# Kernel optimization log

Measured on AMD Instinct MI355X. Metric: run time of the kernel, lower is better.

## Reference

```python
import jax, jax.numpy as jnp
import numpy as np

H, W, C = 192, 192, 1024

def setup_inputs() -> dict:
    key = jax.random.key(0)
    k1, k2 = jax.random.split(key)
    x = jax.random.normal(k1, (1, H, W, C), dtype=jnp.float32)
    gamma = jax.random.normal(k2, (1,), dtype=jnp.float32)
    return {"x": x, "gamma": gamma}

def reference(x, gamma):
    b, h, w, c = x.shape
    # NOTE: faithful to the TF code: a pure reshape of NHWC into (1, C, H*W),
    # with NO transpose (the original relies on reshape semantics).
    proj = x.reshape(1, c, h * w)                      # query == key^T == value
    energy = jnp.einsum('bcn,bdn->bcd', proj, proj)    # (1, C, C)
    energy_new = jnp.max(energy, axis=-1, keepdims=True) - energy  # sign-flipped
    attention = jax.nn.softmax(energy_new, axis=-1)    # (1, C, C)
    out = jnp.einsum('bcd,bdn->bcn', attention, proj)  # (1, C, H*W)
    out = out.reshape(1, h, w, c)
    return gamma * out + x
```

## Files before the change

### kernel.cpp

```cpp
#include <hip/hip_runtime.h>
#include <cstdint>

#define C_DIM 1024
#define N_DIM 36864

typedef unsigned short ushort_t;
typedef __attribute__((ext_vector_type(8))) short bf16x8;
typedef __attribute__((ext_vector_type(4))) float f32x4;

__device__ __forceinline__ ushort_t f2b(float f) {
    unsigned u = __float_as_uint(f);
    u = (u + 0x7fffu + ((u >> 16) & 1u)) >> 16;
    return (ushort_t)u;
}
__device__ __forceinline__ float b2f(ushort_t b) {
    return __uint_as_float(((unsigned)b) << 16);
}

__device__ __forceinline__ void async16(const void* g, const void* lds) {
    __builtin_amdgcn_global_load_lds(
        (const __attribute__((address_space(1))) unsigned int*)(uintptr_t)g,
        (__attribute__((address_space(3))) unsigned int*)(uint32_t)(uintptr_t)lds,
        16, 0, 0);
}

__global__ __launch_bounds__(256) void k_convert(const float* __restrict__ x,
                                                 ushort_t* __restrict__ ph,
                                                 ushort_t* __restrict__ pl) {
    int i = blockIdx.x * 256 + threadIdx.x;
    float4 v = ((const float4*)x)[i];
    ushort4 h, l;
    h.x = f2b(v.x); l.x = f2b(v.x - b2f(h.x));
    h.y = f2b(v.y); l.y = f2b(v.y - b2f(h.y));
    h.z = f2b(v.z); l.z = f2b(v.z - b2f(h.z));
    h.w = f2b(v.w); l.w = f2b(v.w - b2f(h.w));
    ((ushort4*)ph)[i] = h;
    ((ushort4*)pl)[i] = l;
}

__global__ __launch_bounds__(256) void k_convtrans(const float* __restrict__ x,
                                                   ushort_t* __restrict__ ph,
                                                   ushort_t* __restrict__ pl,
                                                   ushort_t* __restrict__ pht) {
    __shared__ __align__(16) ushort_t th[64][72];
    const int t = threadIdx.x;
    const int i = t >> 2, qd = t & 3;
    const int c0 = blockIdx.y << 6;
    const size_t n0 = (size_t)blockIdx.x << 6;

    const size_t row = (size_t)(c0 + i) * N_DIM + n0 + (qd << 4);
    const float* src = x + row;
    union { ushort_t s[16]; uint4 q[2]; } H, Lo;
#pragma unroll
    for (int u4 = 0; u4 < 4; ++u4) {
        float4 v = ((const float4*)src)[u4];
        ushort_t h0 = f2b(v.x), h1 = f2b(v.y), h2 = f2b(v.z), h3 = f2b(v.w);
        H.s[u4 * 4 + 0] = h0; Lo.s[u4 * 4 + 0] = f2b(v.x - b2f(h0));
        H.s[u4 * 4 + 1] = h1; Lo.s[u4 * 4 + 1] = f2b(v.y - b2f(h1));
        H.s[u4 * 4 + 2] = h2; Lo.s[u4 * 4 + 2] = f2b(v.z - b2f(h2));
        H.s[u4 * 4 + 3] = h3; Lo.s[u4 * 4 + 3] = f2b(v.w - b2f(h3));
    }
    *(uint4*)(ph + row)     = H.q[0];
    *(uint4*)(ph + row + 8) = H.q[1];
    *(uint4*)(pl + row)     = Lo.q[0];
    *(uint4*)(pl + row + 8) = Lo.q[1];
    *(uint4*)&th[i][qd << 4]       = H.q[0];
    *(uint4*)&th[i][(qd << 4) + 8] = H.q[1];
    __syncthreads();

    ushort_t tmp[16];
#pragma unroll
    for (int u = 0; u < 16; ++u) tmp[u] = th[(qd << 4) + u][i];
    ushort_t* dst = pht + (n0 + i) * C_DIM + c0 + (qd << 4);
    *(uint4*)dst       = *(uint4*)tmp;
    *(uint4*)(dst + 8) = *(uint4*)(tmp + 8);
}

__global__ __launch_bounds__(256) void k_egemm(const ushort_t* __restrict__ ph,
                                               const ushort_t* __restrict__ pl,
                                               float* __restrict__ g1,
                                               float* __restrict__ g2,
                                               int kchunk) {
    __shared__ __align__(16) ushort_t sA [2][128 * 32];
    __shared__ __align__(16) ushort_t sBh[2][64 * 32];
    __shared__ __align__(16) ushort_t sBl[2][64 * 32];

    const int t = threadIdx.x;
    const int w = t >> 6;
    const int L = t & 63;
    const int c0 = blockIdx.x << 7;
    const int d0 = blockIdx.y << 6;
    const int kb = blockIdx.z * kchunk;
    const int lrow = L >> 2, lcol = (L & 3) << 3;

    const ushort_t* gA0 = ph + (size_t)(c0 + (w << 5) + lrow) * N_DIM + kb + lcol;
    const ushort_t* gB0 = (w < 2 ? ph : pl) +
                          (size_t)(d0 + ((w & 1) << 5) + lrow) * N_DIM + kb + lcol;
    ushort_t* lA[2] = { sA[0] + ((w << 5) << 5), sA[1] + ((w << 5) << 5) };
    ushort_t* lB[2] = { (w < 2 ? sBh[0] : sBl[0]) + (((w & 1) << 5) << 5),
                        (w < 2 ? sBh[1] : sBl[1]) + (((w & 1) << 5) << 5) };

    const int wm = (w >> 1) << 6;
    const int wn = (w & 1) << 5;
    const int lm = L & 15, q = L >> 4;

    f32x4 acc1[4][2], acc2[4][2];
#pragma unroll
    for (int a = 0; a < 4; ++a)
#pragma unroll
        for (int b = 0; b < 2; ++b) { acc1[a][b] = (f32x4)0.0f; acc2[a][b] = (f32x4)0.0f; }

    auto stage = [&](int ti, int b) {
        const ushort_t* ga = gA0 + (ti << 5);
        const ushort_t* gb = gB0 + (ti << 5);
        async16(ga,              lA[b]);
        async16(ga + 16 * N_DIM, lA[b] + 16 * 32);
        async16(gb,              lB[b]);
        async16(gb + 16 * N_DIM, lB[b] + 16 * 32);
    };

    const int nIter = kchunk >> 5;
    stage(0, 0);

    for (int ti = 0; ti < nIter; ++ti) {
        const int cb = ti & 1;
        if (ti + 1 < nIter) {
            stage(ti + 1, cb ^ 1);
            __builtin_amdgcn_s_waitcnt(0x0F74);
        } else {
            __builtin_amdgcn_s_waitcnt(0x0F70);
        }
        __builtin_amdgcn_s_barrier();

        bf16x8 a[4], bh[2], bl[2];
#pragma unroll
        for (int mt = 0; mt < 4; ++mt)
            a[mt] = *(const bf16x8*)(sA[cb] + ((wm + (mt << 4) + lm) << 5) + (q << 3));
#pragma unroll
        for (int nt = 0; nt < 2; ++nt) {
            bh[nt] = *(const bf16x8*)(sBh[cb] + ((wn + (nt << 4) + lm) << 5) + (q << 3));
            bl[nt] = *(const bf16x8*)(sBl[cb] + ((wn + (nt << 4) + lm) << 5) + (q << 3));
        }
#pragma unroll
        for (int mt = 0; mt < 4; ++mt)
#pragma unroll
            for (int nt = 0; nt < 2; ++nt) {
                acc1[mt][nt] = __builtin_amdgcn_mfma_f32_16x16x32_bf16(a[mt], bh[nt], acc1[mt][nt], 0, 0, 0);
                acc2[mt][nt] = __builtin_amdgcn_mfma_f32_16x16x32_bf16(a[mt], bl[nt], acc2[mt][nt], 0, 0, 0);
            }
        __builtin_amdgcn_s_barrier();
    }

    const size_t zb = (size_t)blockIdx.z << 20;
#pragma unroll
    for (int mt = 0; mt < 4; ++mt)
#pragma unroll
        for (int nt = 0; nt < 2; ++nt)
#pragma unroll
            for (int r = 0; r < 4; ++r) {
                int cg = c0 + wm + (mt << 4) + (q << 2) + r;
                int dg = d0 + wn + (nt << 4) + lm;
                size_t o = zb + ((size_t)cg << 10) + dg;
                g1[o] = acc1[mt][nt][r];
                g2[o] = acc2[mt][nt][r];
            }
}

__global__ __launch_bounds__(256) void k_reduce(const float* __restrict__ g1,
                                                const float* __restrict__ g2,
                                                float* __restrict__ E,
                                                int splitk) {
    __shared__ float ld[64][65];
    const int t = threadIdx.x;
    const int i = t >> 2;
    const int jb = (t & 3) << 4;
    const int c0 = blockIdx.y << 6;
    const int d0 = blockIdx.x << 6;

    float acc[16];
#pragma unroll
    for (int u = 0; u < 16; ++u) acc[u] = 0.0f;

    for (int z = 0; z < splitk; ++z) {
        const size_t zb = (size_t)z << 20;
        const float* p1 = g1 + zb + ((size_t)(c0 + i) << 10) + d0 + jb;
        const float* p2 = g2 + zb + ((size_t)(c0 + i) << 10) + d0 + jb;
        const float* pt = g2 + zb + ((size_t)(d0 + i) << 10) + c0 + jb;
#pragma unroll
        for (int u4 = 0; u4 < 4; ++u4) {
            float4 v1 = ((const float4*)p1)[u4];
            float4 v2 = ((const float4*)p2)[u4];
            acc[u4 * 4 + 0] += v1.x + v2.x;
            acc[u4 * 4 + 1] += v1.y + v2.y;
            acc[u4 * 4 + 2] += v1.z + v2.z;
            acc[u4 * 4 + 3] += v1.w + v2.w;
        }
        __syncthreads();
#pragma unroll
        for (int u4 = 0; u4 < 4; ++u4)
            *(float4*)&ld[i][jb + u4 * 4] = ((const float4*)pt)[u4];
        __syncthreads();
#pragma unroll
        for (int u = 0; u < 16; ++u)
            acc[u] += ld[jb + u][i];
    }

    float* eo = E + ((size_t)(c0 + i) << 10) + d0 + jb;
#pragma unroll
    for (int u4 = 0; u4 < 4; ++u4) {
        float4 v;
        v.x = acc[u4 * 4 + 0]; v.y = acc[u4 * 4 + 1];
        v.z = acc[u4 * 4 + 2]; v.w = acc[u4 * 4 + 3];
        ((float4*)eo)[u4] = v;
    }
}

__global__ __launch_bounds__(256) void k_softmax(const float* __restrict__ E,
                                                 ushort_t* __restrict__ att) {
    const int c = blockIdx.x;
    const int t = threadIdx.x;
    __shared__ float red[4];
    __shared__ float bcast;

    float4 e4 = ((const float4*)E)[((size_t)c << 8) + t];
    float m = fminf(fminf(e4.x, e4.y), fminf(e4.z, e4.w));
#pragma unroll
    for (int off = 32; off > 0; off >>= 1) m = fminf(m, __shfl_down(m, off));
    if ((t & 63) == 0) red[t >> 6] = m;
    __syncthreads();
    if (t == 0) bcast = fminf(fminf(red[0], red[1]), fminf(red[2], red[3]));
    __syncthreads();
    m = bcast;

    float w0 = expf(m - e4.x), w1 = expf(m - e4.y);
    float w2 = expf(m - e4.z), w3 = expf(m - e4.w);
    float s = w0 + w1 + w2 + w3;
#pragma unroll
    for (int off = 32; off > 0; off >>= 1) s += __shfl_down(s, off);
    if ((t & 63) == 0) red[t >> 6] = s;
    __syncthreads();
    if (t == 0) bcast = red[0] + red[1] + red[2] + red[3];
    __syncthreads();
    float inv = 1.0f / bcast;
    ushort4 o;
    o.x = f2b(w0 * inv); o.y = f2b(w1 * inv);
    o.z = f2b(w2 * inv); o.w = f2b(w3 * inv);
    ((ushort4*)att)[((size_t)c << 8) + t] = o;
}

__global__ __launch_bounds__(256) void k_transpose(const ushort_t* __restrict__ ph,
                                                   ushort_t* __restrict__ pht) {
    __shared__ __align__(16) ushort_t tile[64][72];
    const int t = threadIdx.x;
    const int i = t >> 2, qd = t & 3;
    const int c0 = blockIdx.y << 6;
    const size_t n0 = (size_t)blockIdx.x << 6;

    const ushort_t* src = ph + (size_t)(c0 + i) * N_DIM + n0 + (qd << 4);
    uint4 v0 = *(const uint4*)src;
    uint4 v1 = *(const uint4*)(src + 8);
    *(uint4*)&tile[i][qd << 4]       = v0;
    *(uint4*)&tile[i][(qd << 4) + 8] = v1;
    __syncthreads();

    ushort_t tmp[16];
#pragma unroll
    for (int u = 0; u < 16; ++u) tmp[u] = tile[(qd << 4) + u][i];
    ushort_t* dst = pht + (n0 + i) * C_DIM + c0 + (qd << 4);
    *(uint4*)dst       = *(uint4*)tmp;
    *(uint4*)(dst + 8) = *(uint4*)(tmp + 8);
}

__global__ __launch_bounds__(256) void k_ogemm(const ushort_t* __restrict__ att,
                                               const ushort_t* __restrict__ pht,
                                               const float* __restrict__ x,
                                               const float* __restrict__ gamma,
                                               float* __restrict__ out) {
    __shared__ __align__(16) ushort_t sA[128 * 32];
    __shared__ __align__(16) ushort_t sB[128 * 32];

    const int t = threadIdx.x;
    const int w = t >> 6, L = t & 63;
    const int n0 = blockIdx.x << 7;
    const int c0 = blockIdx.y << 7;
    const int srow = L >> 2, scol = (L & 3) << 3;

    const int wm = (w >> 1) << 6, wn = (w & 1) << 6;
    const int lm = L & 15, q = L >> 4;

    f32x4 acc[4][4];
#pragma unroll
    for (int a = 0; a < 4; ++a)
#pragma unroll
        for (int b = 0; b < 4; ++b) acc[a][b] = (f32x4)0.0f;

    for (int k = 0; k < C_DIM; k += 32) {
#pragma unroll
        for (int j = 0; j < 4; ++j) {
            int ch = (w << 2) + j;
            int row = ((ch & 7) << 4) + srow;
            const ushort_t* src = (ch < 8)
                ? att + (size_t)(c0 + row) * C_DIM + k + scol
                : pht + (size_t)(n0 + row) * C_DIM + k + scol;
            ushort_t* base = (ch < 8) ? sA : sB;
            async16(src, base + (((ch & 7) << 4) << 5));
        }
        __syncthreads();

        bf16x8 a[4], b[4];
#pragma unroll
        for (int mt = 0; mt < 4; ++mt)
            a[mt] = *(const bf16x8*)(sA + ((wm + (mt << 4) + lm) << 5) + (q << 3));
#pragma unroll
        for (int nt = 0; nt < 4; ++nt)
            b[nt] = *(const bf16x8*)(sB + ((wn + (nt << 4) + lm) << 5) + (q << 3));
#pragma unroll
        for (int mt = 0; mt < 4; ++mt)
#pragma unroll
            for (int nt = 0; nt < 4; ++nt)
                acc[mt][nt] = __builtin_amdgcn_mfma_f32_16x16x32_bf16(a[mt], b[nt], acc[mt][nt], 0, 0, 0);
        __syncthreads();
    }

    const float g = gamma[0];
#pragma unroll
    for (int mt = 0; mt < 4; ++mt)
#pragma unroll
        for (int nt = 0; nt < 4; ++nt)
#pragma unroll
            for (int r = 0; r < 4; ++r) {
                int cg = c0 + wm + (mt << 4) + (q << 2) + r;
                int ng = n0 + wn + (nt << 4) + lm;
                size_t o = (size_t)cg * N_DIM + ng;
                out[o] = g * acc[mt][nt][r] + x[o];
            }
}

extern "C" void kernel_launch(void* const* d_in, const int* in_sizes, int n_in,
                              void* d_out, int out_size, void* d_ws, size_t ws_size,
                              hipStream_t stream) {
    const float* x     = (const float*)d_in[0];
    const float* gamma = (const float*)d_in[1];
    float* out = (float*)d_out;
    char* ws = (char*)d_ws;

    const size_t P = 75497472ull, SL = 4194304ull, EB = 4194304ull, AT = 2097152ull;

    int S = 8;
    bool fused = (ws_size >= 3 * P + (size_t)S * 2 * SL + EB + AT);
    if (!fused) {
        if (ws_size < 2 * P + (size_t)S * 2 * SL + EB + AT) S = 4;
        if (ws_size < 2 * P + (size_t)S * 2 * SL + EB + AT) S = 3;
    }
    const int kchunk = N_DIM / S;

    if (fused) {
        ushort_t* ph  = (ushort_t*)(ws);
        ushort_t* pl  = (ushort_t*)(ws + P);
        ushort_t* pht = (ushort_t*)(ws + 2 * P);
        float*    g1  = (float*)   (ws + 3 * P);
        float*    g2  = (float*)   (ws + 3 * P + (size_t)S * SL);
        float*    E   = (float*)   (ws + 3 * P + (size_t)S * 2 * SL);
        ushort_t* att = (ushort_t*)(ws + 3 * P + (size_t)S * 2 * SL + EB);

        k_convtrans<<<dim3(N_DIM / 64, C_DIM / 64), 256, 0, stream>>>(x, ph, pl, pht);
        k_egemm<<<dim3(8, 16, S), 256, 0, stream>>>(ph, pl, g1, g2, kchunk);
        k_reduce<<<dim3(16, 16), 256, 0, stream>>>(g1, g2, E, S);
        k_softmax<<<dim3(C_DIM), 256, 0, stream>>>(E, att);
        k_ogemm<<<dim3(N_DIM / 128, C_DIM / 128), 256, 0, stream>>>(att, pht, x, gamma, out);
    } else {
        ushort_t* ph  = (ushort_t*)(ws);
        ushort_t* pl  = (ushort_t*)(ws + P);
        float*    g1  = (float*)   (ws + 2 * P);
        float*    g2  = (float*)   (ws + 2 * P + (size_t)S * SL);
        float*    E   = (float*)   (ws + 2 * P + (size_t)S * 2 * SL);
        ushort_t* att = (ushort_t*)(ws + 2 * P + (size_t)S * 2 * SL + EB);
        ushort_t* pht = pl;

        k_convert<<<dim3((C_DIM * (size_t)N_DIM / 4) / 256), 256, 0, stream>>>(x, ph, pl);
        k_egemm<<<dim3(8, 16, S), 256, 0, stream>>>(ph, pl, g1, g2, kchunk);
        k_reduce<<<dim3(16, 16), 256, 0, stream>>>(g1, g2, E, S);
        k_softmax<<<dim3(C_DIM), 256, 0, stream>>>(E, att);
        k_transpose<<<dim3(N_DIM / 64, C_DIM / 64), 256, 0, stream>>>(ph, pht);
        k_ogemm<<<dim3(N_DIM / 128, C_DIM / 128), 256, 0, stream>>>(att, pht, x, gamma, out);
    }
}
```

Before: 682.1 us.

## Enlarge energy GEMM tile to 128x128 and XOR-swizzle LDS layout in both GEMMs

The energy GEMM tile grows from 128x64 to 128x128 per block, with separate high and low B buffers each loaded by all four waves. This halves the grid in y and doubles the MFMA work per LDS fill, which improves data reuse. Both GEMMs now use an XOR swizzle on the 16-byte column chunk, applied in the global-to-LDS async copies and in the fragment reads, to cut LDS bank conflicts. The cost is higher LDS use (about 48KB per block) and twice as many accumulator registers, which may lower occupancy. There are also fewer blocks for the split-K grid.

```diff
diff --git a/kernel.cpp b/kernel.cpp
--- a/kernel.cpp
+++ b/kernel.cpp
@@ -23,6 +23,7 @@
         (__attribute__((address_space(3))) unsigned int*)(uint32_t)(uintptr_t)lds,
         16, 0, 0);
 }
+
 
 __global__ __launch_bounds__(256) void k_convert(const float* __restrict__ x,
                                                  ushort_t* __restrict__ ph,
@@ -76,47 +77,52 @@
     *(uint4*)(dst + 8) = *(uint4*)(tmp + 8);
 }
 
-__global__ __launch_bounds__(256) void k_egemm(const ushort_t* __restrict__ ph,
-                                               const ushort_t* __restrict__ pl,
-                                               float* __restrict__ g1,
-                                               float* __restrict__ g2,
-                                               int kchunk) {
+__global__ __launch_bounds__(256, 2) void k_egemm(const ushort_t* __restrict__ ph,
+                                                  const ushort_t* __restrict__ pl,
+                                                  float* __restrict__ g1,
+                                                  float* __restrict__ g2,
+                                                  int kchunk) {
     __shared__ __align__(16) ushort_t sA [2][128 * 32];
-    __shared__ __align__(16) ushort_t sBh[2][64 * 32];
-    __shared__ __align__(16) ushort_t sBl[2][64 * 32];
+    __shared__ __align__(16) ushort_t sBh[2][128 * 32];
+    __shared__ __align__(16) ushort_t sBl[2][128 * 32];
 
     const int t = threadIdx.x;
     const int w = t >> 6;
     const int L = t & 63;
     const int c0 = blockIdx.x << 7;
-    const int d0 = blockIdx.y << 6;
+    const int d0 = blockIdx.y << 7;
     const int kb = blockIdx.z * kchunk;
-    const int lrow = L >> 2, lcol = (L & 3) << 3;
+    const int lrow = L >> 2;
+    const int lcol = (((L & 3) ^ ((L >> 3) & 3)) << 3);
 
     const ushort_t* gA0 = ph + (size_t)(c0 + (w << 5) + lrow) * N_DIM + kb + lcol;
-    const ushort_t* gB0 = (w < 2 ? ph : pl) +
-                          (size_t)(d0 + ((w & 1) << 5) + lrow) * N_DIM + kb + lcol;
-    ushort_t* lA[2] = { sA[0] + ((w << 5) << 5), sA[1] + ((w << 5) << 5) };
-    ushort_t* lB[2] = { (w < 2 ? sBh[0] : sBl[0]) + (((w & 1) << 5) << 5),
-                        (w < 2 ? sBh[1] : sBl[1]) + (((w & 1) << 5) << 5) };
+    const ushort_t* gH0 = ph + (size_t)(d0 + (w << 5) + lrow) * N_DIM + kb + lcol;
+    const ushort_t* gL0 = pl + (size_t)(d0 + (w << 5) + lrow) * N_DIM + kb + lcol;
+    ushort_t* lA[2] = { sA[0]  + (w << 10), sA[1]  + (w << 10) };
+    ushort_t* lH[2] = { sBh[0] + (w << 10), sBh[1] + (w << 10) };
+    ushort_t* lL[2] = { sBl[0] + (w << 10), sBl[1] + (w << 10) };
 
     const int wm = (w >> 1) << 6;
-    const int wn = (w & 1) << 5;
+    const int wn = (w & 1) << 6;
     const int lm = L & 15, q = L >> 4;
-
-    f32x4 acc1[4][2], acc2[4][2];
+    const int co = ((q ^ ((lm >> 1) & 3)) << 3);
+
+    f32x4 acc1[4][4], acc2[4][4];
 #pragma unroll
     for (int a = 0; a < 4; ++a)
 #pragma unroll
-        for (int b = 0; b < 2; ++b) { acc1[a][b] = (f32x4)0.0f; acc2[a][b] = (f32x4)0.0f; }
+        for (int b = 0; b < 4; ++b) { acc1[a][b] = (f32x4)0.0f; acc2[a][b] = (f32x4)0.0f; }
 
     auto stage = [&](int ti, int b) {
         const ushort_t* ga = gA0 + (ti << 5);
-        const ushort_t* gb = gB0 + (ti << 5);
+        const ushort_t* gh = gH0 + (ti << 5);
+        const ushort_t* gl = gL0 + (ti << 5);
         async16(ga,              lA[b]);
-        async16(ga + 16 * N_DIM, lA[b] + 16 * 32);
-        async16(gb,              lB[b]);
-        async16(gb + 16 * N_DIM, lB[b] + 16 * 32);
+        async16(ga + 16 * N_DIM, lA[b] + 512);
+        async16(gh,              lH[b]);
+        async16(gh + 16 * N_DIM, lH[b] + 512);
+        async16(gl,              lL[b]);
+        async16(gl + 16 * N_DIM, lL[b] + 512);
     };
 
     const int nIter = kchunk >> 5;
@@ -126,25 +132,25 @@
         const int cb = ti & 1;
         if (ti + 1 < nIter) {
             stage(ti + 1, cb ^ 1);
-            __builtin_amdgcn_s_waitcnt(0x0F74);
+            __builtin_amdgcn_s_waitcnt(0x0F76);
         } else {
             __builtin_amdgcn_s_waitcnt(0x0F70);
         }
         __builtin_amdgcn_s_barrier();
 
-        bf16x8 a[4], bh[2], bl[2];
+        bf16x8 a[4], bh[4], bl[4];
 #pragma unroll
         for (int mt = 0; mt < 4; ++mt)
-            a[mt] = *(const bf16x8*)(sA[cb] + ((wm + (mt << 4) + lm) << 5) + (q << 3));
-#pragma unroll
-        for (int nt = 0; nt < 2; ++nt) {
-            bh[nt] = *(const bf16x8*)(sBh[cb] + ((wn + (nt << 4) + lm) << 5) + (q << 3));
-            bl[nt] = *(const bf16x8*)(sBl[cb] + ((wn + (nt << 4) + lm) << 5) + (q << 3));
+            a[mt] = *(const bf16x8*)(sA[cb] + ((wm + (mt << 4) + lm) << 5) + co);
+#pragma unroll
+        for (int nt = 0; nt < 4; ++nt) {
+            bh[nt] = *(const bf16x8*)(sBh[cb] + ((wn + (nt << 4) + lm) << 5) + co);
+            bl[nt] = *(const bf16x8*)(sBl[cb] + ((wn + (nt << 4) + lm) << 5) + co);
         }
 #pragma unroll
         for (int mt = 0; mt < 4; ++mt)
 #pragma unroll
-            for (int nt = 0; nt < 2; ++nt) {
+            for (int nt = 0; nt < 4; ++nt) {
                 acc1[mt][nt] = __builtin_amdgcn_mfma_f32_16x16x32_bf16(a[mt], bh[nt], acc1[mt][nt], 0, 0, 0);
                 acc2[mt][nt] = __builtin_amdgcn_mfma_f32_16x16x32_bf16(a[mt], bl[nt], acc2[mt][nt], 0, 0, 0);
             }
@@ -155,7 +161,7 @@
 #pragma unroll
     for (int mt = 0; mt < 4; ++mt)
 #pragma unroll
-        for (int nt = 0; nt < 2; ++nt)
+        for (int nt = 0; nt < 4; ++nt)
 #pragma unroll
             for (int r = 0; r < 4; ++r) {
                 int cg = c0 + wm + (mt << 4) + (q << 2) + r;
@@ -283,10 +289,12 @@
     const int w = t >> 6, L = t & 63;
     const int n0 = blockIdx.x << 7;
     const int c0 = blockIdx.y << 7;
-    const int srow = L >> 2, scol = (L & 3) << 3;
+    const int srow = L >> 2;
+    const int scol = (((L & 3) ^ ((L >> 3) & 3)) << 3);
 
     const int wm = (w >> 1) << 6, wn = (w & 1) << 6;
     const int lm = L & 15, q = L >> 4;
+    const int co = ((q ^ ((lm >> 1) & 3)) << 3);
 
     f32x4 acc[4][4];
 #pragma unroll
@@ -310,10 +318,10 @@
         bf16x8 a[4], b[4];
 #pragma unroll
         for (int mt = 0; mt < 4; ++mt)
-            a[mt] = *(const bf16x8*)(sA + ((wm + (mt << 4) + lm) << 5) + (q << 3));
+            a[mt] = *(const bf16x8*)(sA + ((wm + (mt << 4) + lm) << 5) + co);
 #pragma unroll
         for (int nt = 0; nt < 4; ++nt)
-            b[nt] = *(const bf16x8*)(sB + ((wn + (nt << 4) + lm) << 5) + (q << 3));
+            b[nt] = *(const bf16x8*)(sB + ((wn + (nt << 4) + lm) << 5) + co);
 #pragma unroll
         for (int mt = 0; mt < 4; ++mt)
 #pragma unroll
@@ -364,7 +372,7 @@
         ushort_t* att = (ushort_t*)(ws + 3 * P + (size_t)S * 2 * SL + EB);
 
         k_convtrans<<<dim3(N_DIM / 64, C_DIM / 64), 256, 0, stream>>>(x, ph, pl, pht);
-        k_egemm<<<dim3(8, 16, S), 256, 0, stream>>>(ph, pl, g1, g2, kchunk);
+        k_egemm<<<dim3(8, 8, S), 256, 0, stream>>>(ph, pl, g1, g2, kchunk);
         k_reduce<<<dim3(16, 16), 256, 0, stream>>>(g1, g2, E, S);
         k_softmax<<<dim3(C_DIM), 256, 0, stream>>>(E, att);
         k_ogemm<<<dim3(N_DIM / 128, C_DIM / 128), 256, 0, stream>>>(att, pht, x, gamma, out);
@@ -378,7 +386,7 @@
         ushort_t* pht = pl;
 
         k_convert<<<dim3((C_DIM * (size_t)N_DIM / 4) / 256), 256, 0, stream>>>(x, ph, pl);
-        k_egemm<<<dim3(8, 16, S), 256, 0, stream>>>(ph, pl, g1, g2, kchunk);
+        k_egemm<<<dim3(8, 8, S), 256, 0, stream>>>(ph, pl, g1, g2, kchunk);
         k_reduce<<<dim3(16, 16), 256, 0, stream>>>(g1, g2, E, S);
         k_softmax<<<dim3(C_DIM), 256, 0, stream>>>(E, att);
         k_transpose<<<dim3(N_DIM / 64, C_DIM / 64), 256, 0, stream>>>(ph, pht);
```

Measured after the change: 666.1 us. 2.4% less time.
